# Kernel tuning notes

Measured on AMD Instinct MI355X. Metric: run time of the kernel, lower is better.

## Reference

```python
import jax, jax.numpy as jnp
import numpy as np

B, H, W, C, D = 32, 28, 28, 768, 64  # batch, height, width, input_dim, adapter dim
EMB = 64  # meta_net output / layer_embedding size


def qgelu(x):
    return x * jax.nn.sigmoid(1.702 * x)


def setup_inputs() -> dict:
    key = jax.random.key(0)
    ks = jax.random.split(key, 10)
    s = 0.02
    return {
        "x": jax.random.normal(ks[0], (B, H, W, C), jnp.float32),
        "meta_w1": jax.random.normal(ks[1], (EMB, C), jnp.float32) * s,
        "meta_b1": jnp.zeros((EMB,), jnp.float32),
        "meta_w2": jax.random.normal(ks[2], (EMB, EMB), jnp.float32) * s,
        "meta_b2": jnp.zeros((EMB,), jnp.float32),
        "layer_emb": jax.random.normal(ks[3], (EMB,), jnp.float32),
        "hyper_w": jax.random.normal(ks[4], (D * D * 9, EMB), jnp.float32) * s,
        "hyper_b": jnp.zeros((D * D * 9,), jnp.float32),
        "down_w": jax.random.normal(ks[5], (D, C), jnp.float32) * np.sqrt(6.0 / (C + D)),
        "down_b": jnp.zeros((D,), jnp.float32),
        "up_w": jax.random.normal(ks[6], (C, D), jnp.float32) * s,  # torch inits zeros; random for nontrivial test
        "up_b": jnp.zeros((C,), jnp.float32),
    }


def reference(x, meta_w1, meta_b1, meta_w2, meta_b2, layer_emb,
              hyper_w, hyper_b, down_w, down_b, up_w, up_b):
    # meta_net: Linear -> ReLU -> Linear, then mean over (H, W)
    h = jax.nn.relu(jnp.einsum('bhwc,oc->bhwo', x, meta_w1) + meta_b1)
    prompt = (jnp.einsum('bhwo,po->bhwp', h, meta_w2) + meta_b2).mean(axis=(1, 2))  # [B, EMB]
    # fuse_type == 'add'
    fused = layer_emb[None, :] + prompt  # [B, EMB]
    # hypernet -> per-sample conv weights [B, D, D, 3, 3]
    conv_w = (fused @ hyper_w.T + hyper_b).reshape(-1, D, D, 3, 3)
    # adapter_down + QuickGELU
    x_down = jnp.einsum('bhwc,dc->bhwd', x, down_w) + down_b  # [B,H,W,D]
    x_patch = qgelu(x_down).transpose(0, 3, 1, 2)  # [B,D,H,W]
    # per-sample 3x3 conv, stride 1, padding 1 (vmapped over batch)
    def conv1(xi, wi):
        return jax.lax.conv_general_dilated(xi[None], wi, (1, 1), [(1, 1), (1, 1)])[0]
    y = jax.vmap(conv1)(x_patch, conv_w)  # [B,D,H,W]
    y = qgelu(y.transpose(0, 2, 3, 1))  # [B,H,W,D]; dropout is identity in eval
    return jnp.einsum('bhwd,cd->bhwc', y, up_w) + up_b
```

## Files before the change

kernel.cpp:

```cpp
#include <hip/hip_runtime.h>
#include <math.h>

#define B_    32
#define H_    28
#define W_    28
#define C_    768
#define D_    64
#define EMB_  64
#define HW_   (H_ * W_)
#define NPOS  (B_ * HW_)
#define CWROWS (D_ * D_ * 9)

typedef __attribute__((ext_vector_type(8))) short bf16x8;
typedef __attribute__((ext_vector_type(4))) float f32x4;

__device__ __forceinline__ float qgelu(float v) {
    return v / (1.f + __expf(-1.702f * v));
}
__device__ __forceinline__ float relu(float v) { return fmaxf(v, 0.f); }

__device__ __forceinline__ ushort f2bf(float f) {
    union { float f; unsigned u; } v; v.f = f;
    return (ushort)((v.u + 0x7fffu + ((v.u >> 16) & 1u)) >> 16);
}

__device__ __forceinline__ void* swz(void* base, int row, int kbyte) {
    return (void*)((char*)base + row * 128 + (kbyte ^ ((row & 7) << 4)));
}

typedef const __attribute__((address_space(1))) void g_void;
typedef __attribute__((address_space(3))) void l_void;
__device__ __forceinline__ void gload16(const void* g, void* l) {
    __builtin_amdgcn_global_load_lds((g_void*)g, (l_void*)l, 16, 0, 0);
}

__global__ void k_cvt(const float* __restrict__ w1, const float* __restrict__ dw,
                      const float* __restrict__ uw,
                      ushort* __restrict__ wcat2, ushort* __restrict__ wup2)
{
    const int f = (blockIdx.x * 256 + threadIdx.x) * 4;
    float4 v;
    size_t dst;
    ushort* base;
    if (f < 98304) {
        int n, k;
        if (f < 49152) { n = f / 768;            k = f % 768; v = *(const float4*)(w1 + (size_t)n * 768 + k); }
        else           { int g = f - 49152; n = 64 + g / 768; k = g % 768; v = *(const float4*)(dw + (size_t)(n - 64) * 768 + k); }
        const int kb = k >> 6, kk = k & 63;
        dst  = (size_t)kb * 8192 + n * 64 + (kk ^ ((n & 7) << 3));
        base = wcat2;
    } else {
        const int g = f - 98304;
        const int n = g >> 6, kk = g & 63;
        v = *(const float4*)(uw + g);
        dst  = (size_t)n * 64 + (kk ^ ((n & 7) << 3));
        base = wup2;
    }
    union { ushort u[4]; uint2 p; } o;
    o.u[0] = f2bf(v.x); o.u[1] = f2bf(v.y); o.u[2] = f2bf(v.z); o.u[3] = f2bf(v.w);
    *(uint2*)(base + dst) = o.p;
}

__global__ __launch_bounds__(256)
void k_gemm_md(const float* __restrict__ x, const ushort* __restrict__ wcat2,
               const float* __restrict__ b1, const float* __restrict__ db,
               float* __restrict__ hbuf, ushort* __restrict__ xact)
{
    __shared__ ushort As[32 * 64];
    __shared__ ushort Bs[128 * 64];
    const int t = threadIdx.x;
    const int wid = t >> 6, lane = t & 63;
    const int lo = lane & 15, hi = lane >> 4;
    const int bm = blockIdx.x;

    f32x4 acc[2][2] = {};

    const int arow = t >> 3, akq = t & 7;
    const float* asrc = x + (size_t)(bm * 32 + arow) * C_ + akq * 8;

    float4 p0 = *(const float4*)(asrc);
    float4 p1 = *(const float4*)(asrc + 4);

    for (int k0 = 0; k0 < C_; k0 += 64) {
        __syncthreads();
        {
            union { ushort u[8]; float4 v; } tmp;
            tmp.u[0] = f2bf(p0.x); tmp.u[1] = f2bf(p0.y);
            tmp.u[2] = f2bf(p0.z); tmp.u[3] = f2bf(p0.w);
            tmp.u[4] = f2bf(p1.x); tmp.u[5] = f2bf(p1.y);
            tmp.u[6] = f2bf(p1.z); tmp.u[7] = f2bf(p1.w);
            *(float4*)swz(As, arow, akq * 16) = tmp.v;
        }
        {
            const ushort* bsrc = wcat2 + (size_t)(k0 >> 6) * 8192;
            #pragma unroll
            for (int c = 0; c < 4; ++c) {
                const int cbase = (wid * 4 + c) * 512;
                gload16(bsrc + cbase + lane * 8, (ushort*)Bs + cbase);
            }
        }
        if (k0 + 64 < C_) {
            p0 = *(const float4*)(asrc + k0 + 64);
            p1 = *(const float4*)(asrc + k0 + 68);
        }
        __syncthreads();

        #pragma unroll
        for (int ks = 0; ks < 2; ++ks) {
            bf16x8 a[2], b[2];
            #pragma unroll
            for (int i = 0; i < 2; ++i)
                a[i] = *(const bf16x8*)swz(As, i * 16 + lo, ks * 64 + hi * 16);
            #pragma unroll
            for (int j = 0; j < 2; ++j)
                b[j] = *(const bf16x8*)swz(Bs, wid * 32 + j * 16 + lo, ks * 64 + hi * 16);
            #pragma unroll
            for (int i = 0; i < 2; ++i)
                #pragma unroll
                for (int j = 0; j < 2; ++j)
                    acc[i][j] = __builtin_amdgcn_mfma_f32_16x16x32_bf16(a[i], b[j], acc[i][j], 0, 0, 0);
        }
    }

    #pragma unroll
    for (int j = 0; j < 2; ++j) {
        const int n = wid * 32 + j * 16 + lo;
        if (n < 64) {
            const float bias = b1[n];
            #pragma unroll
            for (int i = 0; i < 2; ++i)
                #pragma unroll
                for (int r = 0; r < 4; ++r) {
                    int pos = bm * 32 + i * 16 + hi * 4 + r;
                    hbuf[(size_t)pos * 64 + n] = relu(acc[i][j][r] + bias);
                }
        } else {
            const float bias = db[n - 64];
            #pragma unroll
            for (int i = 0; i < 2; ++i)
                #pragma unroll
                for (int r = 0; r < 4; ++r) {
                    int pos = bm * 32 + i * 16 + hi * 4 + r;
                    xact[(size_t)pos * 64 + (n - 64)] = f2bf(qgelu(acc[i][j][r] + bias));
                }
        }
    }
}

__global__ void k_reduce1(const float* __restrict__ hbuf, float* __restrict__ partial)
{
    __shared__ float part[16][EMB_];
    const int b = blockIdx.x, q = blockIdx.y;
    const int tid = threadIdx.x;
    const int e4 = tid & 15, pc = tid >> 4;

    const float* base = hbuf + ((size_t)b * HW_ + q * 196) * 64 + e4 * 4;
    float4 acc = make_float4(0.f, 0.f, 0.f, 0.f);
    for (int i = pc; i < 196; i += 16) {
        float4 v = *(const float4*)(base + (size_t)i * 64);
        acc.x += v.x; acc.y += v.y; acc.z += v.z; acc.w += v.w;
    }
    part[pc][e4 * 4 + 0] = acc.x;
    part[pc][e4 * 4 + 1] = acc.y;
    part[pc][e4 * 4 + 2] = acc.z;
    part[pc][e4 * 4 + 3] = acc.w;
    __syncthreads();
    if (tid < EMB_) {
        float s = 0.f;
        #pragma unroll
        for (int c = 0; c < 16; ++c) s += part[c][tid];
        partial[(size_t)(b * 4 + q) * EMB_ + tid] = s;
    }
}

__global__ void k_reduce2(const float* __restrict__ partial,
                          const float* __restrict__ w2, const float* __restrict__ b2,
                          float* __restrict__ prompt)
{
    __shared__ float hm[EMB_];
    const int b = blockIdx.x;
    const int e = threadIdx.x;
    float s = partial[(size_t)(b * 4 + 0) * EMB_ + e]
            + partial[(size_t)(b * 4 + 1) * EMB_ + e]
            + partial[(size_t)(b * 4 + 2) * EMB_ + e]
            + partial[(size_t)(b * 4 + 3) * EMB_ + e];
    hm[e] = s * (1.f / HW_);
    __syncthreads();
    const float4* w2r = (const float4*)(w2 + (size_t)e * EMB_);
    const float4* hm4 = (const float4*)hm;
    float a0 = 0.f, a1 = 0.f, a2 = 0.f, a3 = 0.f;
    #pragma unroll
    for (int i = 0; i < EMB_ / 4; ++i) {
        float4 h = hm4[i], w = w2r[i];
        a0 = fmaf(h.x, w.x, a0); a1 = fmaf(h.y, w.y, a1);
        a2 = fmaf(h.z, w.z, a2); a3 = fmaf(h.w, w.w, a3);
    }
    prompt[b * EMB_ + e] = (a0 + a1) + (a2 + a3) + b2[e];
}

__global__ void k_hyper(const float* __restrict__ prompt, const float* __restrict__ layer_emb,
                        const float* __restrict__ hyper_w, const float* __restrict__ hyper_b,
                        ushort* __restrict__ cwb)
{
    __shared__ float fused[B_][EMB_];
    const int tid = threadIdx.x;
    for (int i = tid; i < B_ * EMB_; i += 256) {
        int e = i & (EMB_ - 1);
        fused[i >> 6][e] = layer_emb[e] + prompt[i];
    }
    __syncthreads();

    const int f    = blockIdx.x * 256 + tid;
    const int din  = f & 63;
    const int dout = (f >> 6) & 63;
    const int tap  = f >> 12;
    const int r    = (dout * 64 + din) * 9 + tap;

    float wrow[EMB_];
    const float4* hw4 = (const float4*)(hyper_w + (size_t)r * EMB_);
    #pragma unroll
    for (int i = 0; i < EMB_ / 4; ++i) {
        float4 v = hw4[i];
        wrow[i*4+0] = v.x; wrow[i*4+1] = v.y; wrow[i*4+2] = v.z; wrow[i*4+3] = v.w;
    }
    const float hb = hyper_b[r];

    const int b0 = blockIdx.y * 8;
    for (int b = b0; b < b0 + 8; ++b) {
        float a0 = 0.f, a1 = 0.f, a2 = 0.f, a3 = 0.f;
        #pragma unroll
        for (int i = 0; i < EMB_; i += 4) {
            a0 = fmaf(fused[b][i+0], wrow[i+0], a0);
            a1 = fmaf(fused[b][i+1], wrow[i+1], a1);
            a2 = fmaf(fused[b][i+2], wrow[i+2], a2);
            a3 = fmaf(fused[b][i+3], wrow[i+3], a3);
        }
        cwb[(size_t)b * CWROWS + f] = f2bf((a0 + a1) + (a2 + a3) + hb);
    }
}

__global__ __launch_bounds__(512)
void k_conv(const ushort* __restrict__ xact, const ushort* __restrict__ cwb,
            ushort* __restrict__ yact)
{
    __shared__ ushort wsl[192 * 64];
    __shared__ ushort xs[34 * 64];
    const int t = threadIdx.x;
    const int lane = t & 63;
    const int lo = lane & 15, hi = lane >> 4;
    const int b = blockIdx.x / H_;
    const int h = blockIdx.x % H_;
    const int mtile = (t >> 6) >> 2;
    const int ntile = (t >> 6) & 3;
    const int w0 = mtile * 16;

    f32x4 acc = {};

    for (int kh = 0; kh < 3; ++kh) {
        const int hh = h + kh - 1;
        __syncthreads();
        const ushort* wsrc = cwb + (size_t)b * CWROWS + (size_t)kh * 3 * 4096;
        #pragma unroll
        for (int s = 0; s < 3; ++s) {
            int j = s * 512 + t;
            *(float4*)swz(wsl, j >> 3, (j & 7) * 16) = *(const float4*)(wsrc + j * 8);
        }
        if (t < 272) {
            int c = t >> 3, kseg = t & 7;
            int w = c - 1;
            float4 v = make_float4(0.f, 0.f, 0.f, 0.f);
            if (hh >= 0 && hh < H_ && w >= 0 && w < W_)
                v = *(const float4*)(xact + ((size_t)((b * H_ + hh) * W_) + w) * 64 + kseg * 8);
            *(float4*)swz(xs, c, kseg * 16) = v;
        }
        __syncthreads();
        #pragma unroll
        for (int kw = 0; kw < 3; ++kw) {
            #pragma unroll
            for (int ks = 0; ks < 2; ++ks) {
                bf16x8 a  = *(const bf16x8*)swz(xs, w0 + lo + kw, ks * 64 + hi * 16);
                bf16x8 bf = *(const bf16x8*)swz(wsl, kw * 64 + ntile * 16 + lo, ks * 64 + hi * 16);
                acc = __builtin_amdgcn_mfma_f32_16x16x32_bf16(a, bf, acc, 0, 0, 0);
            }
        }
    }

    const int dout = ntile * 16 + lo;
    #pragma unroll
    for (int r = 0; r < 4; ++r) {
        int w = w0 + hi * 4 + r;
        if (w < W_)
            yact[((size_t)((b * H_ + h) * W_) + w) * 64 + dout] = f2bf(qgelu(acc[r]));
    }
}

__global__ __launch_bounds__(256)
void k_up(const ushort* __restrict__ yact, const ushort* __restrict__ wup2,
          const float* __restrict__ ub, float* __restrict__ out)
{
    __shared__ ushort As[32 * 64];
    __shared__ ushort Bs[128 * 64];
    const int t = threadIdx.x;
    const int wid = t >> 6, lane = t & 63;
    const int lo = lane & 15, hi = lane >> 4;
    const int bm = blockIdx.x;

    {
        int row = t >> 3, kseg = t & 7;
        *(float4*)swz(As, row, kseg * 16) =
            *(const float4*)(yact + (size_t)(bm * 32 + row) * 64 + kseg * 8);
    }
    __syncthreads();
    bf16x8 af[2][2];
    #pragma unroll
    for (int ks = 0; ks < 2; ++ks)
        #pragma unroll
        for (int i = 0; i < 2; ++i)
            af[ks][i] = *(const bf16x8*)swz(As, i * 16 + lo, ks * 64 + hi * 16);

    for (int nc = 0; nc < 6; ++nc) {
        __syncthreads();
        {
            const ushort* bsrc = wup2 + (size_t)nc * 8192;
            #pragma unroll
            for (int c = 0; c < 4; ++c) {
                const int cbase = (wid * 4 + c) * 512;
                gload16(bsrc + cbase + lane * 8, (ushort*)Bs + cbase);
            }
        }
        __syncthreads();

        f32x4 acc[2][2] = {};
        #pragma unroll
        for (int ks = 0; ks < 2; ++ks) {
            bf16x8 b[2];
            #pragma unroll
            for (int j = 0; j < 2; ++j)
                b[j] = *(const bf16x8*)swz(Bs, wid * 32 + j * 16 + lo, ks * 64 + hi * 16);
            #pragma unroll
            for (int i = 0; i < 2; ++i)
                #pragma unroll
                for (int j = 0; j < 2; ++j)
                    acc[i][j] = __builtin_amdgcn_mfma_f32_16x16x32_bf16(af[ks][i], b[j], acc[i][j], 0, 0, 0);
        }

        #pragma unroll
        for (int j = 0; j < 2; ++j) {
            const int n = nc * 128 + wid * 32 + j * 16 + lo;
            const float bias = ub[n];
            #pragma unroll
            for (int i = 0; i < 2; ++i)
                #pragma unroll
                for (int r = 0; r < 4; ++r) {
                    int pos = bm * 32 + i * 16 + hi * 4 + r;
                    out[(size_t)pos * C_ + n] = acc[i][j][r] + bias;
                }
        }
    }
}

extern "C" void kernel_launch(void* const* d_in, const int* in_sizes, int n_in,
                              void* d_out, int out_size, void* d_ws, size_t ws_size,
                              hipStream_t stream) {
    const float* x         = (const float*)d_in[0];
    const float* meta_w1   = (const float*)d_in[1];
    const float* meta_b1   = (const float*)d_in[2];
    const float* meta_w2   = (const float*)d_in[3];
    const float* meta_b2   = (const float*)d_in[4];
    const float* layer_emb = (const float*)d_in[5];
    const float* hyper_w   = (const float*)d_in[6];
    const float* hyper_b   = (const float*)d_in[7];
    const float* down_w    = (const float*)d_in[8];
    const float* down_b    = (const float*)d_in[9];
    const float* up_w      = (const float*)d_in[10];
    const float* up_b      = (const float*)d_in[11];
    float* out = (float*)d_out;

    char* p = (char*)d_ws;
    float*  hbuf    = (float*)p;           p += (size_t)NPOS * 64 * 4;
    ushort* yact    = (ushort*)hbuf;
    ushort* xact    = (ushort*)p;          p += (size_t)NPOS * 64 * 2;
    float*  prompt  = (float*)p;           p += (size_t)B_ * EMB_ * 4;
    float*  partial = (float*)p;           p += (size_t)B_ * 4 * EMB_ * 4;
    ushort* cwb     = (ushort*)p;          p += (size_t)B_ * CWROWS * 2;
    ushort* wcat2   = (ushort*)p;          p += (size_t)128 * C_ * 2;
    ushort* wup2    = (ushort*)p;

    k_cvt<<<144, 256, 0, stream>>>(meta_w1, down_w, up_w, wcat2, wup2);
    k_gemm_md<<<NPOS / 32, 256, 0, stream>>>(x, wcat2, meta_b1, down_b, hbuf, xact);
    k_reduce1<<<dim3(B_, 4), 256, 0, stream>>>(hbuf, partial);
    k_reduce2<<<B_, 64, 0, stream>>>(partial, meta_w2, meta_b2, prompt);
    dim3 hgrid(CWROWS / 256, B_ / 8);
    k_hyper<<<hgrid, 256, 0, stream>>>(prompt, layer_emb, hyper_w, hyper_b, cwb);
    k_conv<<<B_ * H_, 512, 0, stream>>>(xact, cwb, yact);
    k_up<<<NPOS / 32, 256, 0, stream>>>(yact, wup2, up_b, out);
}
```

Baseline: 73.41 us.

## Fuse reduce2 into hypernet kernel and fuse conv with up-projection

The meta_net second linear (k_reduce2) now runs inside every k_hyper block, recomputing the prompt for its 8 batch rows from partial sums. The 3x3 conv and the up-projection GEMM become one kernel: conv outputs go through QuickGELU into shared memory, and the same block multiplies them by the up weights and writes the final output. This removes two launches and the yact round trip through global memory. In exchange, meta_w2 work is repeated across hyper blocks, and each conv block loops over all 768 output channels with extra barriers and only 28 useful rows out of 32.

```diff
diff --git a/kernel.cpp b/kernel.cpp
--- a/kernel.cpp
+++ b/kernel.cpp
@@ -173,40 +173,40 @@
     }
 }
 
-__global__ void k_reduce2(const float* __restrict__ partial,
-                          const float* __restrict__ w2, const float* __restrict__ b2,
-                          float* __restrict__ prompt)
-{
-    __shared__ float hm[EMB_];
-    const int b = blockIdx.x;
-    const int e = threadIdx.x;
-    float s = partial[(size_t)(b * 4 + 0) * EMB_ + e]
-            + partial[(size_t)(b * 4 + 1) * EMB_ + e]
-            + partial[(size_t)(b * 4 + 2) * EMB_ + e]
-            + partial[(size_t)(b * 4 + 3) * EMB_ + e];
-    hm[e] = s * (1.f / HW_);
-    __syncthreads();
-    const float4* w2r = (const float4*)(w2 + (size_t)e * EMB_);
-    const float4* hm4 = (const float4*)hm;
-    float a0 = 0.f, a1 = 0.f, a2 = 0.f, a3 = 0.f;
-    #pragma unroll
-    for (int i = 0; i < EMB_ / 4; ++i) {
-        float4 h = hm4[i], w = w2r[i];
-        a0 = fmaf(h.x, w.x, a0); a1 = fmaf(h.y, w.y, a1);
-        a2 = fmaf(h.z, w.z, a2); a3 = fmaf(h.w, w.w, a3);
-    }
-    prompt[b * EMB_ + e] = (a0 + a1) + (a2 + a3) + b2[e];
-}
-
-__global__ void k_hyper(const float* __restrict__ prompt, const float* __restrict__ layer_emb,
+__global__ void k_hyper(const float* __restrict__ partial, const float* __restrict__ layer_emb,
+                        const float* __restrict__ w2, const float* __restrict__ b2,
                         const float* __restrict__ hyper_w, const float* __restrict__ hyper_b,
                         ushort* __restrict__ cwb)
 {
-    __shared__ float fused[B_][EMB_];
+    __shared__ float w2L[64][65];
+    __shared__ float hmL[8][EMB_];
+    __shared__ float fusedL[8][EMB_];
     const int tid = threadIdx.x;
-    for (int i = tid; i < B_ * EMB_; i += 256) {
-        int e = i & (EMB_ - 1);
-        fused[i >> 6][e] = layer_emb[e] + prompt[i];
+    const int b0 = blockIdx.y * 8;
+
+    for (int i = tid; i < 1024; i += 256) {
+        int r = i >> 4, c = (i & 15) * 4;
+        float4 v = *(const float4*)(w2 + (size_t)r * 64 + c);
+        w2L[r][c] = v.x; w2L[r][c + 1] = v.y; w2L[r][c + 2] = v.z; w2L[r][c + 3] = v.w;
+    }
+    for (int i = tid; i < 512; i += 256) {
+        int bl = i >> 6, e = i & 63;
+        const float* pp = partial + (size_t)((b0 + bl) * 4) * EMB_ + e;
+        float s = pp[0] + pp[64] + pp[128] + pp[192];
+        hmL[bl][e] = s * (1.f / HW_);
+    }
+    __syncthreads();
+    for (int i = tid; i < 512; i += 256) {
+        int bl = i >> 6, e = i & 63;
+        float a0 = 0.f, a1 = 0.f, a2 = 0.f, a3 = 0.f;
+        #pragma unroll
+        for (int k = 0; k < EMB_; k += 4) {
+            a0 = fmaf(hmL[bl][k + 0], w2L[e][k + 0], a0);
+            a1 = fmaf(hmL[bl][k + 1], w2L[e][k + 1], a1);
+            a2 = fmaf(hmL[bl][k + 2], w2L[e][k + 2], a2);
+            a3 = fmaf(hmL[bl][k + 3], w2L[e][k + 3], a3);
+        }
+        fusedL[bl][e] = (a0 + a1) + (a2 + a3) + b2[e] + layer_emb[e];
     }
     __syncthreads();
 
@@ -225,23 +225,23 @@
     }
     const float hb = hyper_b[r];
 
-    const int b0 = blockIdx.y * 8;
-    for (int b = b0; b < b0 + 8; ++b) {
+    for (int bl = 0; bl < 8; ++bl) {
         float a0 = 0.f, a1 = 0.f, a2 = 0.f, a3 = 0.f;
         #pragma unroll
         for (int i = 0; i < EMB_; i += 4) {
-            a0 = fmaf(fused[b][i+0], wrow[i+0], a0);
-            a1 = fmaf(fused[b][i+1], wrow[i+1], a1);
-            a2 = fmaf(fused[b][i+2], wrow[i+2], a2);
-            a3 = fmaf(fused[b][i+3], wrow[i+3], a3);
-        }
-        cwb[(size_t)b * CWROWS + f] = f2bf((a0 + a1) + (a2 + a3) + hb);
+            a0 = fmaf(fusedL[bl][i+0], wrow[i+0], a0);
+            a1 = fmaf(fusedL[bl][i+1], wrow[i+1], a1);
+            a2 = fmaf(fusedL[bl][i+2], wrow[i+2], a2);
+            a3 = fmaf(fusedL[bl][i+3], wrow[i+3], a3);
+        }
+        cwb[(size_t)(b0 + bl) * CWROWS + f] = f2bf((a0 + a1) + (a2 + a3) + hb);
     }
 }
 
 __global__ __launch_bounds__(512)
-void k_conv(const ushort* __restrict__ xact, const ushort* __restrict__ cwb,
-            ushort* __restrict__ yact)
+void k_convup(const ushort* __restrict__ xact, const ushort* __restrict__ cwb,
+              const ushort* __restrict__ wup2, const float* __restrict__ ub,
+              float* __restrict__ out)
 {
     __shared__ ushort wsl[192 * 64];
     __shared__ ushort xs[34 * 64];
@@ -250,9 +250,9 @@
     const int lo = lane & 15, hi = lane >> 4;
     const int b = blockIdx.x / H_;
     const int h = blockIdx.x % H_;
-    const int mtile = (t >> 6) >> 2;
-    const int ntile = (t >> 6) & 3;
-    const int w0 = mtile * 16;
+    const int mw = (t >> 6) >> 2;
+    const int nw = (t >> 6) & 3;
+    const int w0 = mw * 16;
 
     f32x4 acc = {};
 
@@ -279,83 +279,66 @@
             #pragma unroll
             for (int ks = 0; ks < 2; ++ks) {
                 bf16x8 a  = *(const bf16x8*)swz(xs, w0 + lo + kw, ks * 64 + hi * 16);
-                bf16x8 bf = *(const bf16x8*)swz(wsl, kw * 64 + ntile * 16 + lo, ks * 64 + hi * 16);
+                bf16x8 bf = *(const bf16x8*)swz(wsl, kw * 64 + nw * 16 + lo, ks * 64 + hi * 16);
                 acc = __builtin_amdgcn_mfma_f32_16x16x32_bf16(a, bf, acc, 0, 0, 0);
             }
         }
     }
 
-    const int dout = ntile * 16 + lo;
+    __syncthreads();
+    ushort* yt = xs;
+    const int dout = nw * 16 + lo;
     #pragma unroll
     for (int r = 0; r < 4; ++r) {
         int w = w0 + hi * 4 + r;
-        if (w < W_)
-            yact[((size_t)((b * H_ + h) * W_) + w) * 64 + dout] = f2bf(qgelu(acc[r]));
-    }
-}
-
-__global__ __launch_bounds__(256)
-void k_up(const ushort* __restrict__ yact, const ushort* __restrict__ wup2,
-          const float* __restrict__ ub, float* __restrict__ out)
-{
-    __shared__ ushort As[32 * 64];
-    __shared__ ushort Bs[128 * 64];
-    const int t = threadIdx.x;
-    const int wid = t >> 6, lane = t & 63;
-    const int lo = lane & 15, hi = lane >> 4;
-    const int bm = blockIdx.x;
-
-    {
-        int row = t >> 3, kseg = t & 7;
-        *(float4*)swz(As, row, kseg * 16) =
-            *(const float4*)(yact + (size_t)(bm * 32 + row) * 64 + kseg * 8);
-    }
-    __syncthreads();
-    bf16x8 af[2][2];
+        *(ushort*)swz(yt, w, dout * 2) = f2bf(qgelu(acc[r]));
+    }
+    __syncthreads();
+
+    bf16x8 af[2];
     #pragma unroll
     for (int ks = 0; ks < 2; ++ks)
-        #pragma unroll
-        for (int i = 0; i < 2; ++i)
-            af[ks][i] = *(const bf16x8*)swz(As, i * 16 + lo, ks * 64 + hi * 16);
+        af[ks] = *(const bf16x8*)swz(yt, mw * 16 + lo, ks * 64 + hi * 16);
+
+    ushort* Bs = wsl;
+    const size_t pos0 = (size_t)(b * H_ + h) * W_;
 
     for (int nc = 0; nc < 6; ++nc) {
-        __syncthreads();
         {
             const ushort* bsrc = wup2 + (size_t)nc * 8192;
-            #pragma unroll
-            for (int c = 0; c < 4; ++c) {
-                const int cbase = (wid * 4 + c) * 512;
-                gload16(bsrc + cbase + lane * 8, (ushort*)Bs + cbase);
+            const int wid = t >> 6;
+            #pragma unroll
+            for (int c = 0; c < 2; ++c) {
+                const int cbase = (wid * 2 + c) * 512;
+                gload16(bsrc + cbase + lane * 8, Bs + cbase);
             }
         }
         __syncthreads();
 
-        f32x4 acc[2][2] = {};
+        f32x4 uacc[2] = {};
         #pragma unroll
         for (int ks = 0; ks < 2; ++ks) {
-            bf16x8 b[2];
+            bf16x8 bb[2];
             #pragma unroll
             for (int j = 0; j < 2; ++j)
-                b[j] = *(const bf16x8*)swz(Bs, wid * 32 + j * 16 + lo, ks * 64 + hi * 16);
-            #pragma unroll
-            for (int i = 0; i < 2; ++i)
-                #pragma unroll
-                for (int j = 0; j < 2; ++j)
-                    acc[i][j] = __builtin_amdgcn_mfma_f32_16x16x32_bf16(af[ks][i], b[j], acc[i][j], 0, 0, 0);
+                bb[j] = *(const bf16x8*)swz(Bs, nw * 32 + j * 16 + lo, ks * 64 + hi * 16);
+            #pragma unroll
+            for (int j = 0; j < 2; ++j)
+                uacc[j] = __builtin_amdgcn_mfma_f32_16x16x32_bf16(af[ks], bb[j], uacc[j], 0, 0, 0);
         }
 
         #pragma unroll
         for (int j = 0; j < 2; ++j) {
-            const int n = nc * 128 + wid * 32 + j * 16 + lo;
+            const int n = nc * 128 + nw * 32 + j * 16 + lo;
             const float bias = ub[n];
             #pragma unroll
-            for (int i = 0; i < 2; ++i)
-                #pragma unroll
-                for (int r = 0; r < 4; ++r) {
-                    int pos = bm * 32 + i * 16 + hi * 4 + r;
-                    out[(size_t)pos * C_ + n] = acc[i][j][r] + bias;
-                }
-        }
+            for (int r = 0; r < 4; ++r) {
+                int m = mw * 16 + hi * 4 + r;
+                if (m < W_)
+                    out[(pos0 + m) * C_ + n] = uacc[j][r] + bias;
+            }
+        }
+        __syncthreads();
     }
 }
 
@@ -378,9 +361,7 @@
 
     char* p = (char*)d_ws;
     float*  hbuf    = (float*)p;           p += (size_t)NPOS * 64 * 4;
-    ushort* yact    = (ushort*)hbuf;
     ushort* xact    = (ushort*)p;          p += (size_t)NPOS * 64 * 2;
-    float*  prompt  = (float*)p;           p += (size_t)B_ * EMB_ * 4;
     float*  partial = (float*)p;           p += (size_t)B_ * 4 * EMB_ * 4;
     ushort* cwb     = (ushort*)p;          p += (size_t)B_ * CWROWS * 2;
     ushort* wcat2   = (ushort*)p;          p += (size_t)128 * C_ * 2;
@@ -389,9 +370,8 @@
     k_cvt<<<144, 256, 0, stream>>>(meta_w1, down_w, up_w, wcat2, wup2);
     k_gemm_md<<<NPOS / 32, 256, 0, stream>>>(x, wcat2, meta_b1, down_b, hbuf, xact);
     k_reduce1<<<dim3(B_, 4), 256, 0, stream>>>(hbuf, partial);
-    k_reduce2<<<B_, 64, 0, stream>>>(partial, meta_w2, meta_b2, prompt);
     dim3 hgrid(CWROWS / 256, B_ / 8);
-    k_hyper<<<hgrid, 256, 0, stream>>>(prompt, layer_emb, hyper_w, hyper_b, cwb);
-    k_conv<<<B_ * H_, 512, 0, stream>>>(xact, cwb, yact);
-    k_up<<<NPOS / 32, 256, 0, stream>>>(yact, wup2, up_b, out);
-}
+    k_hyper<<<hgrid, 256, 0, stream>>>(partial, layer_emb, meta_w2, meta_b2,
+                                       hyper_w, hyper_b, cwb);
+    k_convup<<<B_ * H_, 512, 0, stream>>>(xact, cwb, wup2, up_b, out);
+}
```

Result: faster. 70.44 us (-4.1%).
